# Optimization experiments

Measured on AMD Instinct MI355X. Metric: run time of the kernel, lower is better.

## Reference

```python
import jax, jax.numpy as jnp
import numpy as np

N_EMB = 1024
EMB_DIM = 64
COMMITMENT_COST = 2.0


def setup_inputs() -> dict:
    key = jax.random.key(0)
    k1, k2 = jax.random.split(key)
    x = jax.random.normal(k1, (32, 4096, EMB_DIM), dtype=jnp.float32)
    # codebook initialized uniform(-1/K, 1/K) as in the torch module
    W = jax.random.uniform(k2, (N_EMB, EMB_DIM), dtype=jnp.float32,
                           minval=-1.0 / N_EMB, maxval=1.0 / N_EMB)
    return {"x": x, "W": W}


def reference(x, W):
    D = W.shape[1]
    K = W.shape[0]
    # distances computed on detached x (matches x.detach() in torch)
    x_flat = jax.lax.stop_gradient(x).reshape(-1, D)          # [N, D]
    n_tokens = x_flat.shape[0]
    dist = (jnp.sum(W * W, axis=1)[None, :]
            + jnp.sum(x_flat * x_flat, axis=1, keepdims=True)
            - 2.0 * (x_flat @ W.T))                            # [N, K]
    idx = jnp.argmin(dist, axis=1)                             # [N]
    # one-hot @ W == gather
    quantized = W[idx].reshape(x.shape)
    e_latent = jnp.mean((jax.lax.stop_gradient(quantized) - x) ** 2)
    q_latent = jnp.mean((quantized - jax.lax.stop_gradient(x)) ** 2)
    loss = q_latent + COMMITMENT_COST * e_latent
    # straight-through estimator
    quantized_st = x + jax.lax.stop_gradient(quantized - x)
    # codebook stats via scatter-add counts (== encodings.sum(0))
    counts = jnp.zeros((K,), dtype=jnp.float32).at[idx].add(1.0)
    avg_probs = counts / jnp.float32(n_tokens)
    perplexity = jnp.exp(-jnp.sum(avg_probs * jnp.log(avg_probs + 1e-10)))
    usage = jnp.sum(counts >= 1.0).astype(jnp.float32)
    return quantized_st, loss, perplexity, usage
```

## Files before the change

kernel.cpp:

```cpp
#include <hip/hip_runtime.h>


typedef __bf16          bf16x8  __attribute__((ext_vector_type(8)));
typedef float           f32x4   __attribute__((ext_vector_type(4)));
typedef unsigned short  ushortx8 __attribute__((ext_vector_type(8)));

constexpr int D = 64;
constexpr int K = 1024;
constexpr int BLK = 512;
constexpr int TOKB = 512;
constexpr float BIAS = 0.25f;

__device__ __forceinline__ unsigned short f2bf(float f) {
  unsigned u = __builtin_bit_cast(unsigned, f);
  u = (u + 0x7fffu + ((u >> 16) & 1u)) >> 16;
  return (unsigned short)u;
}

__global__ __launch_bounds__(256) void vq_init(const float* __restrict__ W,
                                               unsigned* __restrict__ counts,
                                               float* __restrict__ wph,
                                               double* __restrict__ sse,
                                               unsigned* __restrict__ ticket,
                                               uint4* __restrict__ wswz) {
  const int gid = blockIdx.x * 256 + threadIdx.x;
  const int c = gid >> 3, p = gid & 7;
  const float4* row = reinterpret_cast<const float4*>(W + c * D);
  float4 v0 = row[2 * p], v1 = row[2 * p + 1];
  float s = 0.f;
  s = fmaf(v0.x, v0.x, s); s = fmaf(v0.y, v0.y, s);
  s = fmaf(v0.z, v0.z, s); s = fmaf(v0.w, v0.w, s);
  s = fmaf(v1.x, v1.x, s); s = fmaf(v1.y, v1.y, s);
  s = fmaf(v1.z, v1.z, s); s = fmaf(v1.w, v1.w, s);
  ushortx8 pk;
  pk[0] = f2bf(v0.x); pk[1] = f2bf(v0.y); pk[2] = f2bf(v0.z); pk[3] = f2bf(v0.w);
  pk[4] = f2bf(v1.x); pk[5] = f2bf(v1.y); pk[6] = f2bf(v1.z); pk[7] = f2bf(v1.w);
  const int ct = c >> 4, cnl = c & 15, half = p >> 2, q = p & 3;
  wswz[ct * 128 + half * 64 + q * 16 + cnl] = __builtin_bit_cast(uint4, pk);
  s += __shfl_xor(s, 1, 64);
  s += __shfl_xor(s, 2, 64);
  s += __shfl_xor(s, 4, 64);
  if (p == 0) wph[c] = 0.5f * s;
  if (gid < K) counts[gid] = 0u;
  if (gid == 0) { *sse = 0.0; *ticket = 0u; }
}

__global__ __launch_bounds__(512, 1) void vq_main(const float* __restrict__ x,
                                                  const float* __restrict__ Wf,
                                                  const uint4* __restrict__ wswz,
                                                  const float* __restrict__ wph,
                                                  unsigned* __restrict__ counts,
                                                  double* __restrict__ sse,
                                                  unsigned* __restrict__ ticket,
                                                  float* __restrict__ out,
                                                  int n_tokens) {
  __shared__ uint4 s_w[K * 8];
  __shared__ unsigned s_hist[K];
  __shared__ float s_wphb[K];
  __shared__ unsigned s_idx[TOKB];
  __shared__ float s_red[8];
  __shared__ unsigned s_ured[8];
  __shared__ unsigned s_last;

  const int tid = threadIdx.x;
  const int wv = tid >> 6, lane = tid & 63;
  const int g = lane >> 4, nl = lane & 15;
  const int tokwg = blockIdx.x * TOKB;

#pragma unroll
  for (int r = 0; r < 16; ++r) {
    __builtin_amdgcn_global_load_lds(
        (const __attribute__((address_space(1))) uint4*)(wswz + r * BLK + tid),
        (__attribute__((address_space(3))) uint4*)&s_w[r * BLK + tid],
        16, 0, 0);
  }
  for (int i = tid; i < K; i += BLK) {
    s_hist[i] = 0u;
    s_wphb[i] = wph[i] + BIAS;
  }

  bf16x8 afrag[4][2];
  float xsq = 0.f;
#pragma unroll
  for (int tt = 0; tt < 4; ++tt) {
#pragma unroll
    for (int s = 0; s < 2; ++s) {
      const float* px = x + (size_t)(tokwg + wv * 64 + tt * 16 + nl) * D + s * 32 + g * 8;
      float4 v0 = *reinterpret_cast<const float4*>(px);
      float4 v1 = *reinterpret_cast<const float4*>(px + 4);
      xsq = fmaf(v0.x, v0.x, xsq); xsq = fmaf(v0.y, v0.y, xsq);
      xsq = fmaf(v0.z, v0.z, xsq); xsq = fmaf(v0.w, v0.w, xsq);
      xsq = fmaf(v1.x, v1.x, xsq); xsq = fmaf(v1.y, v1.y, xsq);
      xsq = fmaf(v1.z, v1.z, xsq); xsq = fmaf(v1.w, v1.w, xsq);
      ushortx8 p;
      p[0] = f2bf(v0.x); p[1] = f2bf(v0.y); p[2] = f2bf(v0.z); p[3] = f2bf(v0.w);
      p[4] = f2bf(v1.x); p[5] = f2bf(v1.y); p[6] = f2bf(v1.z); p[7] = f2bf(v1.w);
#pragma unroll
      for (int j = 0; j < 8; ++j) p[j] ^= 0x8000;
      afrag[tt][s] = __builtin_bit_cast(bf16x8, p);
    }
  }

  int key[4][4];
#pragma unroll
  for (int tt = 0; tt < 4; ++tt)
#pragma unroll
    for (int j = 0; j < 4; ++j) key[tt][j] = 0x7fffffff;

  auto process = [&](int ct, uint4 cb0, uint4 cb1) {
    const float w0 = s_wphb[ct * 16 + nl];
    const bf16x8 b0 = __builtin_bit_cast(bf16x8, cb0);
    const bf16x8 b1 = __builtin_bit_cast(bf16x8, cb1);
    const int code0 = ct * 16 + nl;
#pragma unroll
    for (int tt = 0; tt < 4; ++tt) {
      f32x4 acc = (f32x4){w0, w0, w0, w0};
      acc = __builtin_amdgcn_mfma_f32_16x16x32_bf16(afrag[tt][0], b0, acc, 0, 0, 0);
      acc = __builtin_amdgcn_mfma_f32_16x16x32_bf16(afrag[tt][1], b1, acc, 0, 0, 0);
#pragma unroll
      for (int j = 0; j < 4; ++j) {
        const int kb = (int)((__builtin_bit_cast(unsigned, acc[j]) & 0xfffffc00u)
                             | (unsigned)code0);
        if (kb < key[tt][j]) key[tt][j] = kb;
      }
    }
  };

  __syncthreads();

  uint4 c0 = s_w[lane], c1 = s_w[64 + lane];
#pragma unroll 4
  for (int ct = 0; ct < K / 16; ++ct) {
    uint4 n0, n1;
    if (ct + 1 < K / 16) {
      n0 = s_w[(ct + 1) * 128 + lane];
      n1 = s_w[(ct + 1) * 128 + 64 + lane];
    }
    process(ct, c0, c1);
    c0 = n0; c1 = n1;
  }

  float ddist = 0.f;
#pragma unroll
  for (int tt = 0; tt < 4; ++tt) {
#pragma unroll
    for (int j = 0; j < 4; ++j) {
      int k = key[tt][j];
#pragma unroll
      for (int off = 1; off < 16; off <<= 1) {
        const int ok = __shfl_xor(k, off, 64);
        if (ok < k) k = ok;
      }
      if (nl == 0) {
        const unsigned bi = (unsigned)k & 0x3ffu;
        const float d2 = __builtin_bit_cast(float, (unsigned)k & 0xfffffc00u) - BIAS;
        int tl = wv * 64 + tt * 16 + 4 * g + j;
        s_idx[tl] = bi;
        atomicAdd(&s_hist[bi], 1u);
        ddist = fmaf(2.0f, d2, ddist);
      }
    }
  }

  float sv = xsq + ddist;
#pragma unroll
  for (int off = 32; off > 0; off >>= 1) sv += __shfl_down(sv, off, 64);
  if (lane == 0) s_red[wv] = sv;
  __syncthreads();
  if (tid == 0) {
    float t = 0.f;
#pragma unroll
    for (int w = 0; w < 8; ++w) t += s_red[w];
    atomicAdd(sse, (double)t);
  }

  for (int i = tid; i < K; i += BLK) {
    unsigned h = s_hist[i];
    if (h) atomicAdd(&counts[i], h);
  }

  const int d4 = tid & 15;
#pragma unroll
  for (int tk = 0; tk < TOKB / 32; ++tk) {
    int tl = tk * 32 + (tid >> 4);
    unsigned ci = s_idx[tl];
    float4 q = *reinterpret_cast<const float4*>(Wf + ci * D + d4 * 4);
    *reinterpret_cast<float4*>(out + (size_t)(tokwg + tl) * D + d4 * 4) = q;
  }

  __syncthreads();
  if (tid == 0) {
    unsigned t = atomicAdd(ticket, 1u);
    s_last = (t == gridDim.x - 1) ? 1u : 0u;
  }
  __syncthreads();
  if (s_last) {
    const float inv_n = 1.0f / (float)n_tokens;
    float s = 0.f;
    unsigned u = 0;
    for (int c = tid; c < K; c += BLK) {
      unsigned cnt = atomicAdd(&counts[c], 0u);
      float p = (float)cnt * inv_n;
      s += p * logf(p + 1e-10f);
      u += (cnt >= 1u) ? 1u : 0u;
    }
#pragma unroll
    for (int off = 32; off > 0; off >>= 1) {
      s += __shfl_down(s, off, 64);
      u += __shfl_down(u, off, 64);
    }
    if (lane == 0) { s_red[wv] = s; s_ured[wv] = u; }
    __syncthreads();
    if (tid == 0) {
      double sv2 = atomicAdd(sse, 0.0);
      float s2 = 0.f;
      unsigned u2 = 0;
#pragma unroll
      for (int w = 0; w < 8; ++w) { s2 += s_red[w]; u2 += s_ured[w]; }
      double mean = sv2 / ((double)n_tokens * (double)D);
      float* out_tail = out + (size_t)n_tokens * D;
      out_tail[0] = 3.0f * (float)mean;
      out_tail[1] = expf(-s2);
      out_tail[2] = (float)u2;
    }
  }
}

extern "C" void kernel_launch(void* const* d_in, const int* in_sizes, int n_in,
                              void* d_out, int out_size, void* d_ws, size_t ws_size,
                              hipStream_t stream) {
  const float* x = (const float*)d_in[0];
  const float* W = (const float*)d_in[1];
  float* out = (float*)d_out;

  unsigned* counts = (unsigned*)d_ws;
  double* sse = (double*)((char*)d_ws + 4096);
  unsigned* ticket = (unsigned*)((char*)d_ws + 5120);
  float* wph = (float*)((char*)d_ws + 8192);
  uint4* wswz = (uint4*)((char*)d_ws + 16384);

  const int n_tokens = in_sizes[0] / D;
  const int blocks = n_tokens / TOKB;

  vq_init<<<K * 8 / 256, 256, 0, stream>>>(W, counts, wph, sse, ticket, wswz);
  vq_main<<<blocks, BLK, 0, stream>>>(x, W, wswz, wph, counts, sse, ticket,
                                      out, n_tokens);
}
```

Baseline: 107.8 us.

## Split codebook scan across two wave groups per block with LDS min merge

Doubles the block to 1024 threads so two groups of eight waves each scan half of the codebook for the same 512 tokens. Partial argmin keys from the second half are staged in LDS (reusing the codebook buffer) and merged by the first half before the final shuffle reduction. This is meant to raise occupancy and latency hiding per CU, since the grid has only 256 blocks. The cost is duplicate x loads and conversions in both halves, two extra barriers, and the loss of the explicit software prefetch of codebook fragments.

Result: slower. 111.5 us (+3.4%).

```diff
diff --git a/kernel.cpp b/kernel.cpp
--- a/kernel.cpp
+++ b/kernel.cpp
@@ -7,7 +7,7 @@
 
 constexpr int D = 64;
 constexpr int K = 1024;
-constexpr int BLK = 512;
+constexpr int BLK = 1024;
 constexpr int TOKB = 512;
 constexpr float BIAS = 0.25f;
 
@@ -45,38 +45,40 @@
   if (gid == 0) { *sse = 0.0; *ticket = 0u; }
 }
 
-__global__ __launch_bounds__(512, 1) void vq_main(const float* __restrict__ x,
-                                                  const float* __restrict__ Wf,
-                                                  const uint4* __restrict__ wswz,
-                                                  const float* __restrict__ wph,
-                                                  unsigned* __restrict__ counts,
-                                                  double* __restrict__ sse,
-                                                  unsigned* __restrict__ ticket,
-                                                  float* __restrict__ out,
-                                                  int n_tokens) {
+__global__ __launch_bounds__(1024, 1) void vq_main(const float* __restrict__ x,
+                                                   const float* __restrict__ Wf,
+                                                   const uint4* __restrict__ wswz,
+                                                   const float* __restrict__ wph,
+                                                   unsigned* __restrict__ counts,
+                                                   double* __restrict__ sse,
+                                                   unsigned* __restrict__ ticket,
+                                                   float* __restrict__ out,
+                                                   int n_tokens) {
   __shared__ uint4 s_w[K * 8];
   __shared__ unsigned s_hist[K];
   __shared__ float s_wphb[K];
   __shared__ unsigned s_idx[TOKB];
-  __shared__ float s_red[8];
-  __shared__ unsigned s_ured[8];
+  __shared__ float s_red[16];
+  __shared__ unsigned s_ured[16];
   __shared__ unsigned s_last;
 
   const int tid = threadIdx.x;
   const int wv = tid >> 6, lane = tid & 63;
   const int g = lane >> 4, nl = lane & 15;
+  const int tg = wv & 7;
+  const int kh = wv >> 3;
   const int tokwg = blockIdx.x * TOKB;
 
 #pragma unroll
-  for (int r = 0; r < 16; ++r) {
+  for (int r = 0; r < 8; ++r) {
     __builtin_amdgcn_global_load_lds(
         (const __attribute__((address_space(1))) uint4*)(wswz + r * BLK + tid),
         (__attribute__((address_space(3))) uint4*)&s_w[r * BLK + tid],
         16, 0, 0);
   }
-  for (int i = tid; i < K; i += BLK) {
-    s_hist[i] = 0u;
-    s_wphb[i] = wph[i] + BIAS;
+  if (tid < K) {
+    s_hist[tid] = 0u;
+    s_wphb[tid] = wph[tid] + BIAS;
   }
 
   bf16x8 afrag[4][2];
@@ -85,7 +87,7 @@
   for (int tt = 0; tt < 4; ++tt) {
 #pragma unroll
     for (int s = 0; s < 2; ++s) {
-      const float* px = x + (size_t)(tokwg + wv * 64 + tt * 16 + nl) * D + s * 32 + g * 8;
+      const float* px = x + (size_t)(tokwg + tg * 64 + tt * 16 + nl) * D + s * 32 + g * 8;
       float4 v0 = *reinterpret_cast<const float4*>(px);
       float4 v1 = *reinterpret_cast<const float4*>(px + 4);
       xsq = fmaf(v0.x, v0.x, xsq); xsq = fmaf(v0.y, v0.y, xsq);
@@ -107,10 +109,13 @@
 #pragma unroll
     for (int j = 0; j < 4; ++j) key[tt][j] = 0x7fffffff;
 
-  auto process = [&](int ct, uint4 cb0, uint4 cb1) {
+  __syncthreads();
+
+#pragma unroll 4
+  for (int ct = kh * 32; ct < kh * 32 + 32; ++ct) {
     const float w0 = s_wphb[ct * 16 + nl];
-    const bf16x8 b0 = __builtin_bit_cast(bf16x8, cb0);
-    const bf16x8 b1 = __builtin_bit_cast(bf16x8, cb1);
+    const bf16x8 b0 = __builtin_bit_cast(bf16x8, s_w[ct * 128 + lane]);
+    const bf16x8 b1 = __builtin_bit_cast(bf16x8, s_w[ct * 128 + 64 + lane]);
     const int code0 = ct * 16 + nl;
 #pragma unroll
     for (int tt = 0; tt < 4; ++tt) {
@@ -124,45 +129,46 @@
         if (kb < key[tt][j]) key[tt][j] = kb;
       }
     }
-  };
-
-  __syncthreads();
-
-  uint4 c0 = s_w[lane], c1 = s_w[64 + lane];
-#pragma unroll 4
-  for (int ct = 0; ct < K / 16; ++ct) {
-    uint4 n0, n1;
-    if (ct + 1 < K / 16) {
-      n0 = s_w[(ct + 1) * 128 + lane];
-      n1 = s_w[(ct + 1) * 128 + 64 + lane];
-    }
-    process(ct, c0, c1);
-    c0 = n0; c1 = n1;
-  }
+  }
+
+  __syncthreads();
+  int* s_key = (int*)s_w;
+  if (kh == 1) {
+#pragma unroll
+    for (int tt = 0; tt < 4; ++tt)
+#pragma unroll
+      for (int j = 0; j < 4; ++j)
+        s_key[tg * 1024 + (tt * 4 + j) * 64 + lane] = key[tt][j];
+  }
+  __syncthreads();
 
   float ddist = 0.f;
-#pragma unroll
-  for (int tt = 0; tt < 4; ++tt) {
-#pragma unroll
-    for (int j = 0; j < 4; ++j) {
-      int k = key[tt][j];
-#pragma unroll
-      for (int off = 1; off < 16; off <<= 1) {
-        const int ok = __shfl_xor(k, off, 64);
-        if (ok < k) k = ok;
+  if (kh == 0) {
+#pragma unroll
+    for (int tt = 0; tt < 4; ++tt) {
+#pragma unroll
+      for (int j = 0; j < 4; ++j) {
+        int k = key[tt][j];
+        const int ok2 = s_key[tg * 1024 + (tt * 4 + j) * 64 + lane];
+        if (ok2 < k) k = ok2;
+#pragma unroll
+        for (int off = 1; off < 16; off <<= 1) {
+          const int ok = __shfl_xor(k, off, 64);
+          if (ok < k) k = ok;
+        }
+        if (nl == 0) {
+          const unsigned bi = (unsigned)k & 0x3ffu;
+          const float d2 = __builtin_bit_cast(float, (unsigned)k & 0xfffffc00u) - BIAS;
+          int tl = tg * 64 + tt * 16 + 4 * g + j;
+          s_idx[tl] = bi;
+          atomicAdd(&s_hist[bi], 1u);
+          ddist = fmaf(2.0f, d2, ddist);
+        }
       }
-      if (nl == 0) {
-        const unsigned bi = (unsigned)k & 0x3ffu;
-        const float d2 = __builtin_bit_cast(float, (unsigned)k & 0xfffffc00u) - BIAS;
-        int tl = wv * 64 + tt * 16 + 4 * g + j;
-        s_idx[tl] = bi;
-        atomicAdd(&s_hist[bi], 1u);
-        ddist = fmaf(2.0f, d2, ddist);
-      }
-    }
-  }
-
-  float sv = xsq + ddist;
+    }
+  }
+
+  float sv = (kh == 0) ? (xsq + ddist) : 0.f;
 #pragma unroll
   for (int off = 32; off > 0; off >>= 1) sv += __shfl_down(sv, off, 64);
   if (lane == 0) s_red[wv] = sv;
@@ -170,19 +176,19 @@
   if (tid == 0) {
     float t = 0.f;
 #pragma unroll
-    for (int w = 0; w < 8; ++w) t += s_red[w];
+    for (int w = 0; w < 16; ++w) t += s_red[w];
     atomicAdd(sse, (double)t);
   }
 
-  for (int i = tid; i < K; i += BLK) {
-    unsigned h = s_hist[i];
-    if (h) atomicAdd(&counts[i], h);
+  if (tid < K) {
+    unsigned h = s_hist[tid];
+    if (h) atomicAdd(&counts[tid], h);
   }
 
   const int d4 = tid & 15;
 #pragma unroll
-  for (int tk = 0; tk < TOKB / 32; ++tk) {
-    int tl = tk * 32 + (tid >> 4);
+  for (int tk = 0; tk < TOKB / 64; ++tk) {
+    int tl = tk * 64 + (tid >> 4);
     unsigned ci = s_idx[tl];
     float4 q = *reinterpret_cast<const float4*>(Wf + ci * D + d4 * 4);
     *reinterpret_cast<float4*>(out + (size_t)(tokwg + tl) * D + d4 * 4) = q;
@@ -198,11 +204,11 @@
     const float inv_n = 1.0f / (float)n_tokens;
     float s = 0.f;
     unsigned u = 0;
-    for (int c = tid; c < K; c += BLK) {
-      unsigned cnt = atomicAdd(&counts[c], 0u);
+    if (tid < K) {
+      unsigned cnt = atomicAdd(&counts[tid], 0u);
       float p = (float)cnt * inv_n;
-      s += p * logf(p + 1e-10f);
-      u += (cnt >= 1u) ? 1u : 0u;
+      s = p * logf(p + 1e-10f);
+      u = (cnt >= 1u) ? 1u : 0u;
     }
 #pragma unroll
     for (int off = 32; off > 0; off >>= 1) {
@@ -216,7 +222,7 @@
       float s2 = 0.f;
       unsigned u2 = 0;
 #pragma unroll
-      for (int w = 0; w < 8; ++w) { s2 += s_red[w]; u2 += s_ured[w]; }
+      for (int w = 0; w < 16; ++w) { s2 += s_red[w]; u2 += s_ured[w]; }
       double mean = sv2 / ((double)n_tokens * (double)D);
       float* out_tail = out + (size_t)n_tokens * D;
       out_tail[0] = 3.0f * (float)mean;
```
